# Performance work log

Measured on AMD Instinct MI355X. Metric: run time of the kernel, lower is better.

The kernel has to match this reference:

```python
import jax, jax.numpy as jnp
import numpy as np

N_NEURONS, RANK, N_CONV, LY, LX, BATCH = 8192, 1, 64, 36, 36, 256


def setup_inputs() -> dict:
    key = jax.random.key(0)
    k1, k2, k3, k4 = jax.random.split(key, 4)
    conv = jax.random.normal(k1, (BATCH, N_CONV, LY, LX), dtype=jnp.float32)
    Wc = 0.01 * jax.random.normal(k2, (N_NEURONS, RANK, N_CONV), dtype=jnp.float32)
    Wy = 0.01 * jax.random.normal(k3, (N_NEURONS, RANK, LY), dtype=jnp.float32)
    Wx = 0.01 * jax.random.normal(k4, (N_NEURONS, RANK, LX), dtype=jnp.float32)
    bias = jnp.zeros((N_NEURONS,), dtype=jnp.float32)
    return {"conv": conv, "Wc": Wc, "Wy": Wy, "Wx": Wx, "bias": bias}


def reference(conv, Wc, Wy, Wx, bias):
    # yx_separable, rank == 1 path of Readout.forward:
    #   pred = einsum('nrc,nry,icyx,nrx->in', Wc, Wy, conv, Wx)
    #   pred = elu(pred + bias)
    # Staged contraction: build per-neuron rank-1 spatial filter, contract
    # spatial dims first (small y*x=1296), then channels.
    Wyx = jnp.einsum('nry,nrx->nryx', Wy, Wx)              # [N, R, Ly, Lx]
    s = jnp.einsum('icyx,nryx->inrc', conv, Wyx)           # [B, N, R, C]
    pred = jnp.einsum('inrc,nrc->in', s, Wc)               # [B, N]
    return jax.nn.elu(pred + bias)
```

## Files before the change

kernel.cpp:

```cpp
#include <hip/hip_runtime.h>
#include <hip/hip_bf16.h>

#define NNEUR 8192
#define NCONV 64
#define LYC   36
#define LXC   36
#define BATCH 256
#define KRAW  1296
#define KPAD  1344
#define KITER 21
#define MROWS 16384
#define BM 256
#define BN 256
#define BK 64
#define A_IT_H   16384
#define A_TILE_H (KITER * A_IT_H)
#define B_TILE_H (KITER * A_IT_H)

typedef __attribute__((ext_vector_type(8))) _Float16 half8;
typedef __attribute__((ext_vector_type(4))) float f32x4;
typedef __attribute__((ext_vector_type(16))) float f32x16;

__device__ __forceinline__ void async_copy16(const void* g, void* l) {
  __builtin_amdgcn_global_load_lds(
      (const __attribute__((address_space(1))) void*)g,
      (__attribute__((address_space(3))) void*)l, 16, 0, 0);
}

__global__ __launch_bounds__(256) void prep_kernel(
    const float* __restrict__ conv, const float* __restrict__ Wy,
    const float* __restrict__ Wx, _Float16* __restrict__ A,
    _Float16* __restrict__ B) {
  const int t = threadIdx.x;
  const int bx = blockIdx.x;
  const int slot = t & 7;
  half8 h;
  if (bx < 168) {
    const int tile = blockIdx.y;
    const int it = bx >> 3, i = bx & 7;
    const int r = (t >> 3) + 32 * i;
    const int c = (slot - r) & 7;
    const int k0 = it * 64 + c * 8;
    const int grow = tile * BM + r;
    if (k0 < KRAW) {
      const float* s = conv + (size_t)grow * KRAW + k0;
#pragma unroll
      for (int e = 0; e < 8; e++) h[e] = (_Float16)s[e];
    } else {
#pragma unroll
      for (int e = 0; e < 8; e++) h[e] = (_Float16)0.f;
    }
    *(half8*)(A + (size_t)tile * A_TILE_H + ((size_t)bx * 256 + t) * 8) = h;
  } else {
    const int bxp = bx - 168;
    const int it = bxp >> 2, i4 = bxp & 3;
    const int yb = blockIdx.y & 1;
    const int ntile = blockIdx.y >> 1;
    const int r = (t >> 3) + 32 * i4 + 128 * yb;
    const int c = (slot - r) & 7;
    const int k0 = it * 64 + c * 8;
    const int n = ntile * BN + r;
#pragma unroll
    for (int e = 0; e < 8; e++) {
      const int k = k0 + e;
      float v = 0.f;
      if (k < KRAW) {
        const int y = k / LXC;
        const int x = k - y * LXC;
        v = Wy[n * LYC + y] * Wx[n * LXC + x] * 256.f;
      }
      h[e] = (_Float16)v;
    }
    *(half8*)(B + (size_t)ntile * B_TILE_H + (size_t)it * A_IT_H +
              (size_t)(yb * 1024 + i4 * 256 + t) * 8) = h;
  }
}

__global__ __launch_bounds__(512, 2) void gemm_fused_kernel(
    const _Float16* __restrict__ A, const _Float16* __restrict__ B,
    const float* __restrict__ Wc, const float* __restrict__ bias,
    float* __restrict__ out) {
  __shared__ _Float16 As[2][BM * BK];
  __shared__ _Float16 Bs[2][BN * BK];

  const int bid = blockIdx.x;
  const int gid = (bid & 7) * 256 + (bid >> 3);
  const int mtile = gid >> 5;
  const int ntile = gid & 31;
  const int tileN = ntile * BN;

  const int t = threadIdx.x;
  const int lane = t & 63;
  const int wave = t >> 6;
  const int wm = wave >> 2, wn = wave & 3;
  const int r32 = lane & 31, hh = lane >> 5;

  f32x16 acc[4][2] = {};

  const _Float16* pA = A + (size_t)mtile * A_TILE_H + t * 8;
  const _Float16* pB = B + (size_t)ntile * B_TILE_H + t * 8;

  auto stage = [&](int b, int it) {
    const _Float16* sA = pA + it * A_IT_H;
    const _Float16* sB = pB + it * A_IT_H;
    _Float16* lA = &As[b][t * 8];
    _Float16* lB = &Bs[b][t * 8];
#pragma unroll
    for (int i = 0; i < 4; i++) async_copy16(sA + i * 4096, lA + i * 4096);
#pragma unroll
    for (int i = 0; i < 4; i++) async_copy16(sB + i * 4096, lB + i * 4096);
  };

  auto compute = [&](int b) {
#pragma unroll
    for (int ks = 0; ks < 4; ks++) {
      const int cc = 2 * ks + hh;
      half8 bf[2];
#pragma unroll
      for (int nb = 0; nb < 2; nb++) {
        const int r = wn * 64 + nb * 32 + r32;
        bf[nb] = *(const half8*)(&Bs[b][r * 64 + ((cc + r) & 7) * 8]);
      }
      __builtin_amdgcn_s_setprio(1);
#pragma unroll
      for (int mb = 0; mb < 4; mb++) {
        const int r = wm * 128 + mb * 32 + r32;
        const half8 af = *(const half8*)(&As[b][r * 64 + ((cc + r) & 7) * 8]);
#pragma unroll
        for (int nb = 0; nb < 2; nb++)
          acc[mb][nb] = __builtin_amdgcn_mfma_f32_32x32x16_f16(
              af, bf[nb], acc[mb][nb], 0, 0, 0);
      }
      __builtin_amdgcn_s_setprio(0);
    }
  };

  stage(0, 0);
#pragma unroll 1
  for (int it = 0; it < KITER - 1; ++it) {
    stage((it + 1) & 1, it + 1);
    asm volatile("s_waitcnt vmcnt(8)" ::: "memory");
    __builtin_amdgcn_s_barrier();
    compute(it & 1);
    __builtin_amdgcn_s_barrier();
  }
  asm volatile("s_waitcnt vmcnt(0)" ::: "memory");
  __builtin_amdgcn_s_barrier();
  compute((KITER - 1) & 1);

  const int ibase = mtile * 4 + wm * 2;
  float v[2][2];
#pragma unroll
  for (int nb = 0; nb < 2; nb++) {
    const int n_g = tileN + wn * 64 + nb * 32 + r32;
    const float* wc = Wc + (size_t)n_g * NCONV;
    f32x4 w[2][4];
#pragma unroll
    for (int hf = 0; hf < 2; hf++)
#pragma unroll
      for (int g = 0; g < 4; g++)
        w[hf][g] = *(const f32x4*)(wc + hf * 32 + hh * 4 + g * 8);
#pragma unroll
    for (int img = 0; img < 2; img++) {
      float p = 0.f;
#pragma unroll
      for (int hf = 0; hf < 2; hf++)
#pragma unroll
        for (int g = 0; g < 4; g++)
#pragma unroll
          for (int q = 0; q < 4; q++)
            p += acc[img * 2 + hf][nb][g * 4 + q] * w[hf][g][q];
      p += __shfl_xor(p, 32);
      v[img][nb] = p;
    }
  }
  const int img = ibase + hh;
#pragma unroll
  for (int nb = 0; nb < 2; nb++) {
    const int n_out = tileN + wn * 64 + nb * 32 + r32;
    float z = v[hh][nb] * 0.00390625f + bias[n_out];
    z = z > 0.f ? z : (__expf(z) - 1.f);
    out[(size_t)img * NNEUR + n_out] = z;
  }
}

extern "C" void kernel_launch(void* const* d_in, const int* in_sizes, int n_in,
                              void* d_out, int out_size, void* d_ws,
                              size_t ws_size, hipStream_t stream) {
  const float* conv = (const float*)d_in[0];
  const float* Wc = (const float*)d_in[1];
  const float* Wy = (const float*)d_in[2];
  const float* Wx = (const float*)d_in[3];
  const float* bias = (const float*)d_in[4];
  float* out = (float*)d_out;

  _Float16* Abuf = (_Float16*)d_ws;
  _Float16* Bbuf = (_Float16*)((char*)d_ws + (size_t)MROWS * KPAD * 2);

  prep_kernel<<<dim3(252, 64), 256, 0, stream>>>(conv, Wy, Wx, Abuf, Bbuf);
  gemm_fused_kernel<<<2048, 512, 0, stream>>>(Abuf, Bbuf, Wc, bias, out);
}
```

Before: 503.2 us.

## Load B operand directly from global into registers, bypassing LDS

The GEMM stops staging the weight-filter (B) tiles through LDS. Each wave now loads its B fragments straight from global memory into double-buffered registers, one k-step ahead, so only A is staged in LDS. The prep kernel drops the B swizzle to match the new access pattern, the wave grid changes from 2x4 to 4x2, and the block-to-tile mapping keeps four N tiles per XCD so B stays L2-resident. The aim is to cut LDS traffic and footprint, at the cost of exposing global-load latency inside the MFMA loop and sharing vmcnt with the async A copies.

```diff
diff --git a/kernel.cpp b/kernel.cpp
--- a/kernel.cpp
+++ b/kernel.cpp
@@ -57,8 +57,7 @@
     const int yb = blockIdx.y & 1;
     const int ntile = blockIdx.y >> 1;
     const int r = (t >> 3) + 32 * i4 + 128 * yb;
-    const int c = (slot - r) & 7;
-    const int k0 = it * 64 + c * 8;
+    const int k0 = it * 64 + slot * 8;
     const int n = ntile * BN + r;
 #pragma unroll
     for (int e = 0; e < 8; e++) {
@@ -81,106 +80,97 @@
     const float* __restrict__ Wc, const float* __restrict__ bias,
     float* __restrict__ out) {
   __shared__ _Float16 As[2][BM * BK];
-  __shared__ _Float16 Bs[2][BN * BK];
 
   const int bid = blockIdx.x;
-  const int gid = (bid & 7) * 256 + (bid >> 3);
-  const int mtile = gid >> 5;
-  const int ntile = gid & 31;
+  const int xcd = bid & 7, local = bid >> 3;
+  const int ntile = xcd * 4 + (local & 3);
+  const int mtile = local >> 2;
   const int tileN = ntile * BN;
 
   const int t = threadIdx.x;
   const int lane = t & 63;
   const int wave = t >> 6;
-  const int wm = wave >> 2, wn = wave & 3;
+  const int wm = wave >> 1, wn = wave & 1;
   const int r32 = lane & 31, hh = lane >> 5;
 
-  f32x16 acc[4][2] = {};
+  f32x16 acc[2][4] = {};
 
   const _Float16* pA = A + (size_t)mtile * A_TILE_H + t * 8;
-  const _Float16* pB = B + (size_t)ntile * B_TILE_H + t * 8;
+  const _Float16* pB = B + (size_t)ntile * B_TILE_H;
 
   auto stage = [&](int b, int it) {
     const _Float16* sA = pA + it * A_IT_H;
-    const _Float16* sB = pB + it * A_IT_H;
     _Float16* lA = &As[b][t * 8];
-    _Float16* lB = &Bs[b][t * 8];
 #pragma unroll
     for (int i = 0; i < 4; i++) async_copy16(sA + i * 4096, lA + i * 4096);
-#pragma unroll
-    for (int i = 0; i < 4; i++) async_copy16(sB + i * 4096, lB + i * 4096);
   };
 
-  auto compute = [&](int b) {
+  half8 bq[2][4];
+  auto loadB = [&](half8* dst, int it, int ks) {
+    const int cc = 2 * ks + hh;
+    const _Float16* base = pB + (size_t)it * A_IT_H;
 #pragma unroll
-    for (int ks = 0; ks < 4; ks++) {
-      const int cc = 2 * ks + hh;
-      half8 bf[2];
-#pragma unroll
-      for (int nb = 0; nb < 2; nb++) {
-        const int r = wn * 64 + nb * 32 + r32;
-        bf[nb] = *(const half8*)(&Bs[b][r * 64 + ((cc + r) & 7) * 8]);
-      }
-      __builtin_amdgcn_s_setprio(1);
-#pragma unroll
-      for (int mb = 0; mb < 4; mb++) {
-        const int r = wm * 128 + mb * 32 + r32;
-        const half8 af = *(const half8*)(&As[b][r * 64 + ((cc + r) & 7) * 8]);
-#pragma unroll
-        for (int nb = 0; nb < 2; nb++)
-          acc[mb][nb] = __builtin_amdgcn_mfma_f32_32x32x16_f16(
-              af, bf[nb], acc[mb][nb], 0, 0, 0);
-      }
-      __builtin_amdgcn_s_setprio(0);
+    for (int nb = 0; nb < 4; nb++) {
+      const int rb = wn * 128 + nb * 32 + r32;
+      dst[nb] = *(const half8*)(base + (rb * 8 + cc) * 8);
     }
   };
 
   stage(0, 0);
+  loadB(bq[0], 0, 0);
+
 #pragma unroll 1
-  for (int it = 0; it < KITER - 1; ++it) {
-    stage((it + 1) & 1, it + 1);
+  for (int it = 0; it < KITER; ++it) {
+    const int c = it & 1;
+    if (it + 1 < KITER) stage(c ^ 1, it + 1);
     asm volatile("s_waitcnt vmcnt(8)" ::: "memory");
     __builtin_amdgcn_s_barrier();
-    compute(it & 1);
+#pragma unroll
+    for (int ks = 0; ks < 4; ks++) {
+      const int nit = (ks == 3) ? ((it + 1 < KITER) ? it + 1 : it) : it;
+      const int nks = (ks == 3) ? 0 : ks + 1;
+      loadB(bq[(ks + 1) & 1], nit, nks);
+      const int cc = 2 * ks + hh;
+      half8 af[2];
+#pragma unroll
+      for (int mb = 0; mb < 2; mb++) {
+        const int r = wm * 64 + mb * 32 + r32;
+        af[mb] = *(const half8*)(&As[c][r * 64 + ((cc + r) & 7) * 8]);
+      }
+      __builtin_amdgcn_s_setprio(1);
+#pragma unroll
+      for (int mb = 0; mb < 2; mb++)
+#pragma unroll
+        for (int nb = 0; nb < 4; nb++)
+          acc[mb][nb] = __builtin_amdgcn_mfma_f32_32x32x16_f16(
+              af[mb], bq[ks & 1][nb], acc[mb][nb], 0, 0, 0);
+      __builtin_amdgcn_s_setprio(0);
+    }
     __builtin_amdgcn_s_barrier();
   }
-  asm volatile("s_waitcnt vmcnt(0)" ::: "memory");
-  __builtin_amdgcn_s_barrier();
-  compute((KITER - 1) & 1);
 
-  const int ibase = mtile * 4 + wm * 2;
-  float v[2][2];
+  const int img = mtile * 4 + wm;
+  const int nbase = tileN + wn * 128;
 #pragma unroll
-  for (int nb = 0; nb < 2; nb++) {
-    const int n_g = tileN + wn * 64 + nb * 32 + r32;
+  for (int nb = 0; nb < 4; nb++) {
+    const int n_g = nbase + nb * 32 + r32;
     const float* wc = Wc + (size_t)n_g * NCONV;
-    f32x4 w[2][4];
+    float p = 0.f;
 #pragma unroll
-    for (int hf = 0; hf < 2; hf++)
+    for (int mb = 0; mb < 2; mb++)
 #pragma unroll
-      for (int g = 0; g < 4; g++)
-        w[hf][g] = *(const f32x4*)(wc + hf * 32 + hh * 4 + g * 8);
+      for (int g = 0; g < 4; g++) {
+        const f32x4 w = *(const f32x4*)(wc + mb * 32 + hh * 4 + g * 8);
 #pragma unroll
-    for (int img = 0; img < 2; img++) {
-      float p = 0.f;
-#pragma unroll
-      for (int hf = 0; hf < 2; hf++)
-#pragma unroll
-        for (int g = 0; g < 4; g++)
-#pragma unroll
-          for (int q = 0; q < 4; q++)
-            p += acc[img * 2 + hf][nb][g * 4 + q] * w[hf][g][q];
-      p += __shfl_xor(p, 32);
-      v[img][nb] = p;
+        for (int q = 0; q < 4; q++)
+          p += acc[mb][nb][g * 4 + q] * w[q];
+      }
+    p += __shfl_xor(p, 32);
+    if (hh == 0) {
+      float z = p * 0.00390625f + bias[n_g];
+      z = z > 0.f ? z : (__expf(z) - 1.f);
+      out[(size_t)img * NNEUR + n_g] = z;
     }
-  }
-  const int img = ibase + hh;
-#pragma unroll
-  for (int nb = 0; nb < 2; nb++) {
-    const int n_out = tileN + wn * 64 + nb * 32 + r32;
-    float z = v[hh][nb] * 0.00390625f + bias[n_out];
-    z = z > 0.f ? z : (__expf(z) - 1.f);
-    out[(size_t)img * NNEUR + n_out] = z;
   }
 }
 
```

Result: slower. 858.4 us (+70.6%).

## Restructure GEMM k-loop into barrier-separated LDS-load/MFMA phases; incrementalize prep indexing

Applied to the files above, without the earlier changes.

The GEMM main loop is split into four phases per K-tile. Each phase issues all A and B fragment reads from LDS up front, then hits a workgroup barrier and an explicit lgkmcnt(0) wait before a block of eight MFMAs at raised priority, then hits another barrier. The goal is to keep waves in lockstep so LDS reads and MFMA bursts interleave across the two resident workgroups, at the cost of many more barriers per K-tile. The prep kernel also replaces the per-element divide and modulo by 36 with an incrementing (y, x) counter, which removes integer division from the B-operand generation.

```diff
diff --git a/kernel.cpp b/kernel.cpp
--- a/kernel.cpp
+++ b/kernel.cpp
@@ -60,16 +60,17 @@
     const int c = (slot - r) & 7;
     const int k0 = it * 64 + c * 8;
     const int n = ntile * BN + r;
+    const float* wyn = Wy + n * LYC;
+    const float* wxn = Wx + n * LXC;
+    int y = k0 / LXC;
+    int x = k0 - y * LXC;
 #pragma unroll
     for (int e = 0; e < 8; e++) {
       const int k = k0 + e;
       float v = 0.f;
-      if (k < KRAW) {
-        const int y = k / LXC;
-        const int x = k - y * LXC;
-        v = Wy[n * LYC + y] * Wx[n * LXC + x] * 256.f;
-      }
+      if (k < KRAW) v = wyn[y] * wxn[x] * 256.f;
       h[e] = (_Float16)v;
+      if (++x == LXC) { x = 0; ++y; }
     }
     *(half8*)(B + (size_t)ntile * B_TILE_H + (size_t)it * A_IT_H +
               (size_t)(yb * 1024 + i4 * 256 + t) * 8) = h;
@@ -111,42 +112,46 @@
     for (int i = 0; i < 4; i++) async_copy16(sB + i * 4096, lB + i * 4096);
   };
 
-  auto compute = [&](int b) {
-#pragma unroll
-    for (int ks = 0; ks < 4; ks++) {
-      const int cc = 2 * ks + hh;
-      half8 bf[2];
-#pragma unroll
-      for (int nb = 0; nb < 2; nb++) {
-        const int r = wn * 64 + nb * 32 + r32;
-        bf[nb] = *(const half8*)(&Bs[b][r * 64 + ((cc + r) & 7) * 8]);
-      }
-      __builtin_amdgcn_s_setprio(1);
-#pragma unroll
-      for (int mb = 0; mb < 4; mb++) {
-        const int r = wm * 128 + mb * 32 + r32;
-        const half8 af = *(const half8*)(&As[b][r * 64 + ((cc + r) & 7) * 8]);
-#pragma unroll
-        for (int nb = 0; nb < 2; nb++)
-          acc[mb][nb] = __builtin_amdgcn_mfma_f32_32x32x16_f16(
-              af, bf[nb], acc[mb][nb], 0, 0, 0);
-      }
-      __builtin_amdgcn_s_setprio(0);
-    }
+  auto phase = [&](int c, int ks) {
+    const int cc = 2 * ks + hh;
+    half8 bf[2], af[4];
+#pragma unroll
+    for (int nb = 0; nb < 2; nb++) {
+      const int r = wn * 64 + nb * 32 + r32;
+      bf[nb] = *(const half8*)(&Bs[c][r * 64 + ((cc + r) & 7) * 8]);
+    }
+#pragma unroll
+    for (int mb = 0; mb < 4; mb++) {
+      const int r = wm * 128 + mb * 32 + r32;
+      af[mb] = *(const half8*)(&As[c][r * 64 + ((cc + r) & 7) * 8]);
+    }
+    __builtin_amdgcn_s_barrier();
+    asm volatile("s_waitcnt lgkmcnt(0)" ::: "memory");
+    __builtin_amdgcn_s_setprio(1);
+#pragma unroll
+    for (int mb = 0; mb < 4; mb++)
+#pragma unroll
+      for (int nb = 0; nb < 2; nb++)
+        acc[mb][nb] = __builtin_amdgcn_mfma_f32_32x32x16_f16(
+            af[mb], bf[nb], acc[mb][nb], 0, 0, 0);
+    __builtin_amdgcn_s_setprio(0);
+    __builtin_amdgcn_s_barrier();
   };
 
   stage(0, 0);
 #pragma unroll 1
-  for (int it = 0; it < KITER - 1; ++it) {
-    stage((it + 1) & 1, it + 1);
-    asm volatile("s_waitcnt vmcnt(8)" ::: "memory");
+  for (int it = 0; it < KITER; ++it) {
+    const int c = it & 1;
+    if (it + 1 < KITER) {
+      stage(c ^ 1, it + 1);
+      asm volatile("s_waitcnt vmcnt(8)" ::: "memory");
+    } else {
+      asm volatile("s_waitcnt vmcnt(0)" ::: "memory");
+    }
     __builtin_amdgcn_s_barrier();
-    compute(it & 1);
-    __builtin_amdgcn_s_barrier();
-  }
-  asm volatile("s_waitcnt vmcnt(0)" ::: "memory");
-  __builtin_amdgcn_s_barrier();
-  compute((KITER - 1) & 1);
+#pragma unroll
+    for (int ks = 0; ks < 4; ks++) phase(c, ks);
+  }
 
   const int ibase = mtile * 4 + wm * 2;
   float v[2][2];
```

Result: slower. 562.5 us (+11.8%).
